# Performance work log

Hardware: AMD Instinct MI355X
Metric: run time of the kernel (lower is better)

The kernel has to match this reference:

```python
import jax, jax.numpy as jnp
import numpy as np

G, NPG, DEG = 64, 1024, 16          # graphs, nodes/graph, avg degree
N, E = G * NPG, G * NPG * DEG        # 65536 nodes, 1048576 edges
F, H = 128, 128                      # num_features, n_hidden
K1, K2 = NPG // 2, NPG // 4          # ceil(0.5*1024)=512, ceil(0.5*512)=256


def setup_inputs() -> dict:
    key = jax.random.key(0)
    ks = jax.random.split(key, 16)
    x = jax.random.normal(ks[0], (N, F), dtype=jnp.float32)
    # edges constrained within each graph (block-diagonal adjacency)
    offs = (jnp.arange(G, dtype=jnp.int32) * NPG)[:, None]
    src = (jax.random.randint(ks[1], (G, E // G), 0, NPG, dtype=jnp.int32) + offs).reshape(-1)
    dst = (jax.random.randint(ks[2], (G, E // G), 0, NPG, dtype=jnp.int32) + offs).reshape(-1)
    def lin(k, fi, fo):
        s = 1.0 / np.sqrt(fi)
        return jax.random.uniform(k, (fi, fo), jnp.float32, -s, s)
    return dict(
        x=x, src=src, dst=dst,
        W1=lin(ks[3], F, H),  b1=jnp.zeros((H,), jnp.float32),
        Ws1=lin(ks[4], H, 1), bs1=jnp.zeros((1,), jnp.float32),
        W2=lin(ks[5], H, H),  b2=jnp.zeros((H,), jnp.float32),
        Ws2=lin(ks[6], H, 1), bs2=jnp.zeros((1,), jnp.float32),
        Wl1=lin(ks[7], 2 * H, H), bl1=jnp.zeros((H,), jnp.float32),
        Wl2=lin(ks[8], H, 1),     bl2=jnp.zeros((1,), jnp.float32),
    )


def gcn_conv(x, src, dst, ew, W, b):
    """GCNConv: D^-1/2 (A+I) D^-1/2 (x W) + b, with edge weights ew."""
    n = x.shape[0]
    h = x @ W
    loop = jnp.arange(n, dtype=src.dtype)
    s = jnp.concatenate([src, loop])
    d = jnp.concatenate([dst, loop])
    w = jnp.concatenate([ew, jnp.ones((n,), x.dtype)])
    deg = jax.ops.segment_sum(w, d, num_segments=n)
    dinv = jnp.where(deg > 0, jax.lax.rsqrt(jnp.maximum(deg, 1e-12)), 0.0)
    norm = dinv[s] * dinv[d] * w
    return jax.ops.segment_sum(norm[:, None] * h[s], d, num_segments=n) + b


def sag_pool(x, src, dst, ew, Ws, bs, n_per_graph, k):
    """SAGPooling: GCN attention score, per-graph top-k, x*tanh(score), edge prune via mask."""
    n = x.shape[0]
    g = n // n_per_graph
    score = gcn_conv(x, src, dst, ew, Ws, bs)[:, 0]                 # [n]
    _, idx = jax.lax.top_k(score.reshape(g, n_per_graph), k)        # [g, k]
    perm = (idx + (jnp.arange(g, dtype=jnp.int32) * n_per_graph)[:, None]).reshape(-1)
    xn = x[perm] * jnp.tanh(score[perm])[:, None]                   # [g*k, H]
    kept = jnp.zeros((n,), bool).at[perm].set(True)
    nmap = jnp.zeros((n,), jnp.int32).at[perm].set(jnp.arange(g * k, dtype=jnp.int32))
    valid = kept[src] & kept[dst] & (ew > 0)
    ewn = jnp.where(valid, ew, 0.0)
    srcn = jnp.where(valid, nmap[src], 0)
    dstn = jnp.where(valid, nmap[dst], 0)
    return xn, srcn, dstn, ewn


def reference(x, src, dst, W1, b1, Ws1, bs1, W2, b2, Ws2, bs2, Wl1, bl1, Wl2, bl2):
    ew = jnp.ones((src.shape[0],), x.dtype)
    h = jax.nn.relu(gcn_conv(x, src, dst, ew, W1, b1))
    h, s1, d1, ew1 = sag_pool(h, src, dst, ew, Ws1, bs1, NPG, K1)
    hb = h.reshape(G, K1, H)
    x1 = jnp.concatenate([hb.max(axis=1), hb.mean(axis=1)], axis=1)  # [G, 2H]
    h = jax.nn.relu(gcn_conv(h, s1, d1, ew1, W2, b2))
    h, s2, d2, ew2 = sag_pool(h, s1, d1, ew1, Ws2, bs2, K1, K2)
    hb = h.reshape(G, K2, H)
    x2 = jnp.concatenate([hb.max(axis=1), hb.mean(axis=1)], axis=1)
    z = x1 + x2
    z = jax.nn.relu(z @ Wl1 + bl1)                                  # dropout: eval mode (identity)
    return (z @ Wl2 + bl2)[:, 0]                                     # [G]
```

## Files before the change

### kernel.cpp

```cpp
#include <hip/hip_runtime.h>
#include <math.h>

constexpr int NN1 = 65536;
constexpr int EE  = 1048576;
constexpr int GG  = 64;
constexpr int HH  = 128;
constexpr int NPG = 1024;
constexpr int EPG = 16384;
constexpr int K1  = 512;
constexpr int M1  = GG * K1;
constexpr int K2  = 256;
constexpr int M2  = GG * K2;

__device__ __forceinline__ float4 f4add(float4 a, float4 b)
{
    a.x += b.x; a.y += b.y; a.z += b.z; a.w += b.w; return a;
}

__global__ __launch_bounds__(256) void gemm_f32_128(const float* __restrict__ A,
                                                    const float* __restrict__ W,
                                                    const int* __restrict__ rbeg,
                                                    const int* __restrict__ rend,
                                                    float* __restrict__ C)
{
    __shared__ float Wl[64 * 160];
    const int t    = threadIdx.x;
    const int rowg = t >> 3;
    const int cg   = t & 7;
    const int r0   = (blockIdx.x << 7) + rowg;

    const float* Ar0 = A + ((size_t)r0 << 7);
    const float* Ar1 = Ar0 + (32 << 7);
    const float* Ar2 = Ar1 + (32 << 7);
    const float* Ar3 = Ar2 + (32 << 7);

    float acc[4][16];
#pragma unroll
    for (int i = 0; i < 4; ++i)
#pragma unroll
        for (int j = 0; j < 16; ++j) acc[i][j] = 0.f;

    {
        const float4* Wg = (const float4*)W;
#pragma unroll
        for (int i = 0; i < 8; ++i) {
            int idx = t + (i << 8);
            int k   = idx >> 5;
            int c4  = (idx & 31) << 2;
            *(float4*)&Wl[k * 160 + (c4 >> 4) * 20 + (c4 & 15)] = Wg[idx];
        }
    }
    float4 xc0 = *(const float4*)(Ar0), xc1 = *(const float4*)(Ar1);
    float4 xc2 = *(const float4*)(Ar2), xc3 = *(const float4*)(Ar3);
    __syncthreads();

    const float* wbase = &Wl[cg * 20];

#pragma unroll 1
    for (int k0 = 0; k0 < 64; k0 += 4) {
        float4 xn0 = *(const float4*)(Ar0 + k0 + 4);
        float4 xn1 = *(const float4*)(Ar1 + k0 + 4);
        float4 xn2 = *(const float4*)(Ar2 + k0 + 4);
        float4 xn3 = *(const float4*)(Ar3 + k0 + 4);
#pragma unroll
        for (int kk = 0; kk < 4; ++kk) {
            const float* wr = wbase + (k0 + kk) * 160;
            float x0 = ((const float*)&xc0)[kk], x1 = ((const float*)&xc1)[kk];
            float x2 = ((const float*)&xc2)[kk], x3 = ((const float*)&xc3)[kk];
#pragma unroll
            for (int jh = 0; jh < 16; jh += 8) {
                float wv[8];
                *(float4*)&wv[0] = *(const float4*)(wr + jh);
                *(float4*)&wv[4] = *(const float4*)(wr + jh + 4);
#pragma unroll
                for (int j = 0; j < 8; ++j) {
                    acc[0][jh + j] = fmaf(x0, wv[j], acc[0][jh + j]);
                    acc[1][jh + j] = fmaf(x1, wv[j], acc[1][jh + j]);
                    acc[2][jh + j] = fmaf(x2, wv[j], acc[2][jh + j]);
                    acc[3][jh + j] = fmaf(x3, wv[j], acc[3][jh + j]);
                }
            }
        }
        xc0 = xn0; xc1 = xn1; xc2 = xn2; xc3 = xn3;
    }
    __syncthreads();
    {
        const float4* Wg = (const float4*)(W + 64 * 128);
#pragma unroll
        for (int i = 0; i < 8; ++i) {
            int idx = t + (i << 8);
            int k   = idx >> 5;
            int c4  = (idx & 31) << 2;
            *(float4*)&Wl[k * 160 + (c4 >> 4) * 20 + (c4 & 15)] = Wg[idx];
        }
    }
    __syncthreads();

#pragma unroll 1
    for (int k0 = 64; k0 < 128; k0 += 4) {
        bool pf = (k0 < 124);
        float4 xn0, xn1, xn2, xn3;
        if (pf) {
            xn0 = *(const float4*)(Ar0 + k0 + 4);
            xn1 = *(const float4*)(Ar1 + k0 + 4);
            xn2 = *(const float4*)(Ar2 + k0 + 4);
            xn3 = *(const float4*)(Ar3 + k0 + 4);
        }
#pragma unroll
        for (int kk = 0; kk < 4; ++kk) {
            const float* wr = wbase + (k0 - 64 + kk) * 160;
            float x0 = ((const float*)&xc0)[kk], x1 = ((const float*)&xc1)[kk];
            float x2 = ((const float*)&xc2)[kk], x3 = ((const float*)&xc3)[kk];
#pragma unroll
            for (int jh = 0; jh < 16; jh += 8) {
                float wv[8];
                *(float4*)&wv[0] = *(const float4*)(wr + jh);
                *(float4*)&wv[4] = *(const float4*)(wr + jh + 4);
#pragma unroll
                for (int j = 0; j < 8; ++j) {
                    acc[0][jh + j] = fmaf(x0, wv[j], acc[0][jh + j]);
                    acc[1][jh + j] = fmaf(x1, wv[j], acc[1][jh + j]);
                    acc[2][jh + j] = fmaf(x2, wv[j], acc[2][jh + j]);
                    acc[3][jh + j] = fmaf(x3, wv[j], acc[3][jh + j]);
                }
            }
        }
        if (pf) { xc0 = xn0; xc1 = xn1; xc2 = xn2; xc3 = xn3; }
    }

#pragma unroll
    for (int i = 0; i < 4; ++i) {
        int r = r0 + (i << 5);
        float deg = (float)(rend[r] - rbeg[r]) + 1.0f;
        float sc = 1.0f / sqrtf(deg);
        float* cp = C + ((size_t)r << 7) + (cg << 4);
#pragma unroll
        for (int j = 0; j < 16; j += 4) {
            float4 v;
            v.x = acc[i][j] * sc; v.y = acc[i][j + 1] * sc;
            v.z = acc[i][j + 2] * sc; v.w = acc[i][j + 3] * sc;
            *(float4*)(cp + j) = v;
        }
    }
}

__global__ __launch_bounds__(1024) void build_csr1_k(const int* __restrict__ src, const int* __restrict__ dst,
                                                     int* __restrict__ rbeg, int* __restrict__ rend,
                                                     int* __restrict__ csr)
{
    __shared__ int cnt[NPG];
    int t = threadIdx.x, g = blockIdx.x;
    int ebase = g * EPG;
    cnt[t] = 0;
    __syncthreads();
#pragma unroll
    for (int k = 0; k < EPG / 1024; ++k) {
        int d = dst[ebase + t + k * 1024] & (NPG - 1);
        atomicAdd(&cnt[d], 1);
    }
    __syncthreads();
    int deg0 = cnt[t];
    int val = deg0;
    for (int off = 1; off < NPG; off <<= 1) {
        int u = (t >= off) ? cnt[t - off] : 0;
        __syncthreads();
        val += u; cnt[t] = val;
        __syncthreads();
    }
    int node = g * NPG + t;
    rbeg[node] = ebase + val - deg0;
    rend[node] = ebase + val;
    cnt[t] = val - deg0;
    __syncthreads();
#pragma unroll
    for (int k = 0; k < EPG / 1024; ++k) {
        int e = ebase + t + k * 1024;
        int d = dst[e] & (NPG - 1);
        int pos = atomicAdd(&cnt[d], 1);
        csr[ebase + pos] = src[e];
    }
}

__global__ __launch_bounds__(1024) void build_csr2_k(const int* __restrict__ src, const int* __restrict__ dst,
                                                     const int* __restrict__ nmap,
                                                     int* __restrict__ rbeg, int* __restrict__ rend,
                                                     int* __restrict__ csr)
{
    __shared__ int cnt[K1];
    int t = threadIdx.x, g = blockIdx.x;
    int ebase = g * EPG;
    if (t < K1) cnt[t] = 0;
    __syncthreads();
    int ns[EPG / 1024], nd[EPG / 1024];
#pragma unroll
    for (int k = 0; k < EPG / 1024; ++k) {
        int e = ebase + t + k * 1024;
        ns[k] = nmap[src[e]];
        nd[k] = nmap[dst[e]];
        if (ns[k] >= 0 && nd[k] >= 0) atomicAdd(&cnt[nd[k] & (K1 - 1)], 1);
    }
    __syncthreads();
    int deg0 = 0, val = 0;
    if (t < K1) { deg0 = cnt[t]; val = deg0; }
    for (int off = 1; off < K1; off <<= 1) {
        int u = (t < K1 && t >= off) ? cnt[t - off] : 0;
        __syncthreads();
        if (t < K1) { val += u; cnt[t] = val; }
        __syncthreads();
    }
    if (t < K1) {
        int node = g * K1 + t;
        rbeg[node] = ebase + val - deg0;
        rend[node] = ebase + val;
        cnt[t] = val - deg0;
    }
    __syncthreads();
#pragma unroll
    for (int k = 0; k < EPG / 1024; ++k) {
        if (ns[k] >= 0 && nd[k] >= 0) {
            int pos = atomicAdd(&cnt[nd[k] & (K1 - 1)], 1);
            csr[ebase + pos] = ns[k];
        }
    }
}

__global__ __launch_bounds__(256) void agg_feat_k(const float4* __restrict__ XWs,
                                                  const int* __restrict__ rbeg, const int* __restrict__ rend,
                                                  const int* __restrict__ csr,
                                                  const float* __restrict__ bias, const float* __restrict__ Ws,
                                                  float* __restrict__ hout, float* __restrict__ hss, int n)
{
    int nblk = gridDim.x;
    int bid  = blockIdx.x;
    int b    = (bid & 7) * (nblk >> 3) + (bid >> 3);
    int half = threadIdx.x >> 5;
    int lane = threadIdx.x & 31;
    int node = (b << 3) + half;
    if (node >= n) return;
    const float4* Xf = XWs + lane;

    float4 A = make_float4(0.f, 0.f, 0.f, 0.f), B = A, C = A, D = A;
    int p0 = rbeg[node], p1 = rend[node];
    int p = p0;
    for (; p + 8 <= p1; p += 8) {
        int s0 = csr[p], s1 = csr[p + 1], s2 = csr[p + 2], s3 = csr[p + 3];
        int s4 = csr[p + 4], s5 = csr[p + 5], s6 = csr[p + 6], s7 = csr[p + 7];
        float4 v0 = Xf[(size_t)s0 << 5], v1 = Xf[(size_t)s1 << 5];
        float4 v2 = Xf[(size_t)s2 << 5], v3 = Xf[(size_t)s3 << 5];
        float4 v4 = Xf[(size_t)s4 << 5], v5 = Xf[(size_t)s5 << 5];
        float4 v6 = Xf[(size_t)s6 << 5], v7 = Xf[(size_t)s7 << 5];
        A = f4add(A, v0); B = f4add(B, v1); C = f4add(C, v2); D = f4add(D, v3);
        A = f4add(A, v4); B = f4add(B, v5); C = f4add(C, v6); D = f4add(D, v7);
    }
    for (; p + 4 <= p1; p += 4) {
        int s0 = csr[p], s1 = csr[p + 1], s2 = csr[p + 2], s3 = csr[p + 3];
        float4 v0 = Xf[(size_t)s0 << 5], v1 = Xf[(size_t)s1 << 5];
        float4 v2 = Xf[(size_t)s2 << 5], v3 = Xf[(size_t)s3 << 5];
        A = f4add(A, v0); B = f4add(B, v1); C = f4add(C, v2); D = f4add(D, v3);
    }
    for (; p < p1; ++p) {
        int s = csr[p];
        A = f4add(A, Xf[(size_t)s << 5]);
    }
    float4 acc = f4add(f4add(A, B), f4add(C, D));
    acc = f4add(acc, Xf[(size_t)node << 5]);

    float dd = 1.0f / sqrtf((float)(p1 - p0) + 1.0f);
    float4 bb = *(const float4*)(bias + (lane << 2));
    acc.x = fmaxf(fmaf(acc.x, dd, bb.x), 0.f);
    acc.y = fmaxf(fmaf(acc.y, dd, bb.y), 0.f);
    acc.z = fmaxf(fmaf(acc.z, dd, bb.z), 0.f);
    acc.w = fmaxf(fmaf(acc.w, dd, bb.w), 0.f);
    *(float4*)(hout + ((size_t)node << 7) + (lane << 2)) = acc;

    float4 wsv = *(const float4*)(Ws + (lane << 2));
    float pq = acc.x * wsv.x + acc.y * wsv.y + acc.z * wsv.z + acc.w * wsv.w;
#pragma unroll
    for (int off = 16; off > 0; off >>= 1) pq += __shfl_down(pq, off, 32);
    if (lane == 0) hss[node] = dd * pq;
}

template <int NNE, int KK, bool MARK>
__global__ void sctopk_k(const int* __restrict__ rbeg, const int* __restrict__ rend,
                         const int* __restrict__ csr, const float* __restrict__ hss,
                         const float* __restrict__ bsp,
                         int* __restrict__ perm, float* __restrict__ tsel,
                         int* __restrict__ nmap)
{
    __shared__ unsigned long long keys[NNE];
    int t = threadIdx.x, g = blockIdx.x;
    int node = g * NNE + t;
    int p0 = rbeg[node], p1 = rend[node];
    float a = 0.f, b = 0.f, c = 0.f, e = 0.f;
    int p = p0;
    for (; p + 8 <= p1; p += 8) {
        int s0 = csr[p], s1 = csr[p + 1], s2 = csr[p + 2], s3 = csr[p + 3];
        int s4 = csr[p + 4], s5 = csr[p + 5], s6 = csr[p + 6], s7 = csr[p + 7];
        a += hss[s0]; b += hss[s1]; c += hss[s2]; e += hss[s3];
        a += hss[s4]; b += hss[s5]; c += hss[s6]; e += hss[s7];
    }
    for (; p + 4 <= p1; p += 4) {
        int s0 = csr[p], s1 = csr[p + 1], s2 = csr[p + 2], s3 = csr[p + 3];
        a += hss[s0]; b += hss[s1]; c += hss[s2]; e += hss[s3];
    }
    for (; p < p1; ++p) a += hss[csr[p]];
    float dd = 1.0f / sqrtf((float)(p1 - p0) + 1.0f);
    float s = fmaf((a + b) + (c + e) + hss[node], dd, bsp[0]);

    unsigned u = __float_as_uint(s);
    u = (u & 0x80000000u) ? ~u : (u | 0x80000000u);
    keys[t] = (((unsigned long long)u) << 32) | (unsigned)(NNE - 1 - t);
    __syncthreads();
    for (int k = 2; k <= NNE; k <<= 1) {
        for (int j = k >> 1; j > 0; j >>= 1) {
            int ixj = t ^ j;
            if (ixj > t) {
                unsigned long long ka = keys[t], kb = keys[ixj];
                bool up = ((t & k) == 0);
                if ((ka > kb) == up) { keys[t] = kb; keys[ixj] = ka; }
            }
            __syncthreads();
        }
    }
    unsigned long long key = keys[NNE - 1 - t];
    int idx = NNE - 1 - (int)(key & 0xFFFFFFFFu);
    if (t < KK) {
        perm[g * KK + t] = g * NNE + idx;
        unsigned uu = (unsigned)(key >> 32);
        float sc = __uint_as_float((uu & 0x80000000u) ? (uu ^ 0x80000000u) : ~uu);
        tsel[g * KK + t] = tanhf(sc);
        if (MARK) nmap[g * NNE + idx] = g * KK + t;
    } else if (MARK) {
        nmap[g * NNE + idx] = -1;
    }
}

__global__ void gather_k(const float* __restrict__ h, const float* __restrict__ tsel,
                         const int* __restrict__ perm, float* __restrict__ xn)
{
    int nblk = gridDim.x;
    int bid  = blockIdx.x;
    int b    = (bid & 7) * (nblk >> 3) + (bid >> 3);
    int gid = b * 256 + threadIdx.x;
    int node = gid >> 5, f4 = (gid & 31) << 2;
    int o = perm[node];
    float tv = tsel[node];
    float4 v = *(const float4*)(h + ((size_t)o << 7) + f4);
    v.x *= tv; v.y *= tv; v.z *= tv; v.w *= tv;
    *(float4*)(xn + ((size_t)node << 7) + f4) = v;
}

__global__ __launch_bounds__(128) void readout_p_k(const float* __restrict__ xn, float* __restrict__ part)
{
    int b = blockIdx.x, t = threadIdx.x;
    const float* bp = xn + (size_t)b * (128 * 128);
    float mx = -INFINITY, sm = 0.f;
#pragma unroll 4
    for (int r = 0; r < 128; ++r) {
        float v = bp[r * 128 + t];
        mx = fmaxf(mx, v);
        sm += v;
    }
    part[b * 256 + t] = mx;
    part[b * 256 + 128 + t] = sm;
}

__global__ __launch_bounds__(128) void mlp_k(const float* __restrict__ part1, const float* __restrict__ part2,
                                             const float* __restrict__ Wl1, const float* __restrict__ bl1,
                                             const float* __restrict__ Wl2, const float* __restrict__ bl2,
                                             float* __restrict__ out)
{
    __shared__ float z[256];
    __shared__ float red[128];
    int g = blockIdx.x, t = threadIdx.x;
    float mx1 = -INFINITY, sm1 = 0.f;
#pragma unroll
    for (int j = 0; j < 4; ++j) {
        mx1 = fmaxf(mx1, part1[(g * 4 + j) * 256 + t]);
        sm1 += part1[(g * 4 + j) * 256 + 128 + t];
    }
    float mx2 = -INFINITY, sm2 = 0.f;
#pragma unroll
    for (int j = 0; j < 2; ++j) {
        mx2 = fmaxf(mx2, part2[(g * 2 + j) * 256 + t]);
        sm2 += part2[(g * 2 + j) * 256 + 128 + t];
    }
    z[t]       = mx1 + mx2;
    z[t + 128] = sm1 * (1.f / 512.f) + sm2 * (1.f / 256.f);
    __syncthreads();
    float acc = bl1[t];
    for (int k = 0; k < 256; ++k) acc = fmaf(z[k], Wl1[k * 128 + t], acc);
    float zz = fmaxf(acc, 0.f);
    red[t] = zz * Wl2[t];
    __syncthreads();
    for (int off = 64; off > 0; off >>= 1) {
        if (t < off) red[t] += red[t + off];
        __syncthreads();
    }
    if (t == 0) out[g] = red[0] + bl2[0];
}

extern "C" void kernel_launch(void* const* d_in, const int* in_sizes, int n_in,
                              void* d_out, int out_size, void* d_ws, size_t ws_size,
                              hipStream_t stream)
{
    const float* x   = (const float*)d_in[0];
    const int*   src = (const int*)d_in[1];
    const int*   dst = (const int*)d_in[2];
    const float* W1  = (const float*)d_in[3];
    const float* b1  = (const float*)d_in[4];
    const float* Ws1 = (const float*)d_in[5];
    const float* bs1 = (const float*)d_in[6];
    const float* W2  = (const float*)d_in[7];
    const float* b2  = (const float*)d_in[8];
    const float* Ws2 = (const float*)d_in[9];
    const float* bs2 = (const float*)d_in[10];
    const float* Wl1 = (const float*)d_in[11];
    const float* bl1 = (const float*)d_in[12];
    const float* Wl2 = (const float*)d_in[13];
    const float* bl2 = (const float*)d_in[14];
    float* out = (float*)d_out;
    char* ws = (char*)d_ws;

    float* XW1 = (float*)(ws);
    float* h1  = (float*)(ws + ((size_t)32 << 20));
    float* xn  = XW1;
    float* XW2 = (float*)(ws + ((size_t)16 << 20));
    float* h2  = h1;
    float* xn2 = (float*)(ws + ((size_t)48 << 20));
    size_t SB = (size_t)64 << 20;
    auto alloc = [&](size_t bytes) { char* p = ws + SB; SB += (bytes + 255) & ~(size_t)255; return p; };
    int* csr1     = (int*)alloc((size_t)EE * 4);
    int* rbeg1    = (int*)alloc(NN1 * 4);
    int* rend1    = (int*)alloc(NN1 * 4);
    float* hss1   = (float*)alloc(NN1 * 4);
    int* nmap     = (int*)alloc(NN1 * 4);
    int* perm1    = (int*)alloc(M1 * 4);
    float* tsel1  = (float*)alloc(M1 * 4);
    int* rbeg2    = (int*)alloc(M1 * 4);
    int* rend2    = (int*)alloc(M1 * 4);
    float* hss2   = (float*)alloc(M1 * 4);
    int* perm2    = (int*)alloc(M2 * 4);
    float* tsel2  = (float*)alloc(M2 * 4);
    float* part1  = (float*)alloc(256 * 256 * 4);
    float* part2  = (float*)alloc(128 * 256 * 4);
    int* csr2     = csr1;
    (void)ws_size; (void)in_sizes; (void)n_in; (void)out_size;

    build_csr1_k<<<GG, 1024, 0, stream>>>(src, dst, rbeg1, rend1, csr1);
    gemm_f32_128<<<NN1 / 128, 256, 0, stream>>>(x, W1, rbeg1, rend1, XW1);
    agg_feat_k<<<NN1 / 8, 256, 0, stream>>>((const float4*)XW1, rbeg1, rend1, csr1, b1, Ws1, h1, hss1, NN1);
    sctopk_k<NPG, K1, true><<<GG, NPG, 0, stream>>>(rbeg1, rend1, csr1, hss1, bs1, perm1, tsel1, nmap);
    gather_k<<<(M1 * 32) / 256, 256, 0, stream>>>(h1, tsel1, perm1, xn);
    readout_p_k<<<M1 / 128, 128, 0, stream>>>(xn, part1);
    build_csr2_k<<<GG, 1024, 0, stream>>>(src, dst, nmap, rbeg2, rend2, csr2);
    gemm_f32_128<<<M1 / 128, 256, 0, stream>>>(xn, W2, rbeg2, rend2, XW2);
    agg_feat_k<<<M1 / 8, 256, 0, stream>>>((const float4*)XW2, rbeg2, rend2, csr2, b2, Ws2, h2, hss2, M1);
    sctopk_k<K1, K2, false><<<GG, K1, 0, stream>>>(rbeg2, rend2, csr2, hss2, bs2, perm2, tsel2, nullptr);
    gather_k<<<(M2 * 32) / 256, 256, 0, stream>>>(h2, tsel2, perm2, xn2);
    readout_p_k<<<M2 / 128, 128, 0, stream>>>(xn2, part2);
    mlp_k<<<GG, 128, 0, stream>>>(part1, part2, Wl1, bl1, Wl2, bl2, out);
}
```

Measured before the change: 219.5 us.

## Fuse top-k gather and tanh scaling into second GEMM and readout kernels

Removes the standalone gather kernels that materialized the pooled feature matrices. The second-layer GEMM now reads rows of h1 indirectly through perm1 and applies the tanh score factor in its epilogue. The readout kernels also gather through perm and apply tsel on the fly. This saves two launches and a write and reread of the pooled matrices, at the cost of indirect row loads in the GEMM and readout and redundant gathers of h1 by two kernels.

```diff
diff --git a/kernel.cpp b/kernel.cpp
--- a/kernel.cpp
+++ b/kernel.cpp
@@ -17,11 +17,11 @@
     a.x += b.x; a.y += b.y; a.z += b.z; a.w += b.w; return a;
 }
 
-__global__ __launch_bounds__(256) void gemm_f32_128(const float* __restrict__ A,
-                                                    const float* __restrict__ W,
-                                                    const int* __restrict__ rbeg,
-                                                    const int* __restrict__ rend,
-                                                    float* __restrict__ C)
+__global__ __launch_bounds__(256) void gemm1_k(const float* __restrict__ A,
+                                               const float* __restrict__ W,
+                                               const int* __restrict__ rbeg,
+                                               const int* __restrict__ rend,
+                                               float* __restrict__ C)
 {
     __shared__ float Wl[64 * 160];
     const int t    = threadIdx.x;
@@ -133,6 +133,135 @@
         int r = r0 + (i << 5);
         float deg = (float)(rend[r] - rbeg[r]) + 1.0f;
         float sc = 1.0f / sqrtf(deg);
+        float* cp = C + ((size_t)r << 7) + (cg << 4);
+#pragma unroll
+        for (int j = 0; j < 16; j += 4) {
+            float4 v;
+            v.x = acc[i][j] * sc; v.y = acc[i][j + 1] * sc;
+            v.z = acc[i][j + 2] * sc; v.w = acc[i][j + 3] * sc;
+            *(float4*)(cp + j) = v;
+        }
+    }
+}
+
+__global__ __launch_bounds__(256) void gemm2_k(const float* __restrict__ A,
+                                               const float* __restrict__ W,
+                                               const int* __restrict__ rbeg,
+                                               const int* __restrict__ rend,
+                                               const int* __restrict__ perm,
+                                               const float* __restrict__ tsel,
+                                               float* __restrict__ C)
+{
+    __shared__ float Wl[64 * 160];
+    const int t    = threadIdx.x;
+    const int rowg = t >> 3;
+    const int cg   = t & 7;
+    const int r0   = (blockIdx.x << 7) + rowg;
+
+    const float* Ar0 = A + ((size_t)perm[r0] << 7);
+    const float* Ar1 = A + ((size_t)perm[r0 + 32] << 7);
+    const float* Ar2 = A + ((size_t)perm[r0 + 64] << 7);
+    const float* Ar3 = A + ((size_t)perm[r0 + 96] << 7);
+
+    float acc[4][16];
+#pragma unroll
+    for (int i = 0; i < 4; ++i)
+#pragma unroll
+        for (int j = 0; j < 16; ++j) acc[i][j] = 0.f;
+
+    {
+        const float4* Wg = (const float4*)W;
+#pragma unroll
+        for (int i = 0; i < 8; ++i) {
+            int idx = t + (i << 8);
+            int k   = idx >> 5;
+            int c4  = (idx & 31) << 2;
+            *(float4*)&Wl[k * 160 + (c4 >> 4) * 20 + (c4 & 15)] = Wg[idx];
+        }
+    }
+    float4 xc0 = *(const float4*)(Ar0), xc1 = *(const float4*)(Ar1);
+    float4 xc2 = *(const float4*)(Ar2), xc3 = *(const float4*)(Ar3);
+    __syncthreads();
+
+    const float* wbase = &Wl[cg * 20];
+
+#pragma unroll 1
+    for (int k0 = 0; k0 < 64; k0 += 4) {
+        float4 xn0 = *(const float4*)(Ar0 + k0 + 4);
+        float4 xn1 = *(const float4*)(Ar1 + k0 + 4);
+        float4 xn2 = *(const float4*)(Ar2 + k0 + 4);
+        float4 xn3 = *(const float4*)(Ar3 + k0 + 4);
+#pragma unroll
+        for (int kk = 0; kk < 4; ++kk) {
+            const float* wr = wbase + (k0 + kk) * 160;
+            float x0 = ((const float*)&xc0)[kk], x1 = ((const float*)&xc1)[kk];
+            float x2 = ((const float*)&xc2)[kk], x3 = ((const float*)&xc3)[kk];
+#pragma unroll
+            for (int jh = 0; jh < 16; jh += 8) {
+                float wv[8];
+                *(float4*)&wv[0] = *(const float4*)(wr + jh);
+                *(float4*)&wv[4] = *(const float4*)(wr + jh + 4);
+#pragma unroll
+                for (int j = 0; j < 8; ++j) {
+                    acc[0][jh + j] = fmaf(x0, wv[j], acc[0][jh + j]);
+                    acc[1][jh + j] = fmaf(x1, wv[j], acc[1][jh + j]);
+                    acc[2][jh + j] = fmaf(x2, wv[j], acc[2][jh + j]);
+                    acc[3][jh + j] = fmaf(x3, wv[j], acc[3][jh + j]);
+                }
+            }
+        }
+        xc0 = xn0; xc1 = xn1; xc2 = xn2; xc3 = xn3;
+    }
+    __syncthreads();
+    {
+        const float4* Wg = (const float4*)(W + 64 * 128);
+#pragma unroll
+        for (int i = 0; i < 8; ++i) {
+            int idx = t + (i << 8);
+            int k   = idx >> 5;
+            int c4  = (idx & 31) << 2;
+            *(float4*)&Wl[k * 160 + (c4 >> 4) * 20 + (c4 & 15)] = Wg[idx];
+        }
+    }
+    __syncthreads();
+
+#pragma unroll 1
+    for (int k0 = 64; k0 < 128; k0 += 4) {
+        bool pf = (k0 < 124);
+        float4 xn0, xn1, xn2, xn3;
+        if (pf) {
+            xn0 = *(const float4*)(Ar0 + k0 + 4);
+            xn1 = *(const float4*)(Ar1 + k0 + 4);
+            xn2 = *(const float4*)(Ar2 + k0 + 4);
+            xn3 = *(const float4*)(Ar3 + k0 + 4);
+        }
+#pragma unroll
+        for (int kk = 0; kk < 4; ++kk) {
+            const float* wr = wbase + (k0 - 64 + kk) * 160;
+            float x0 = ((const float*)&xc0)[kk], x1 = ((const float*)&xc1)[kk];
+            float x2 = ((const float*)&xc2)[kk], x3 = ((const float*)&xc3)[kk];
+#pragma unroll
+            for (int jh = 0; jh < 16; jh += 8) {
+                float wv[8];
+                *(float4*)&wv[0] = *(const float4*)(wr + jh);
+                *(float4*)&wv[4] = *(const float4*)(wr + jh + 4);
+#pragma unroll
+                for (int j = 0; j < 8; ++j) {
+                    acc[0][jh + j] = fmaf(x0, wv[j], acc[0][jh + j]);
+                    acc[1][jh + j] = fmaf(x1, wv[j], acc[1][jh + j]);
+                    acc[2][jh + j] = fmaf(x2, wv[j], acc[2][jh + j]);
+                    acc[3][jh + j] = fmaf(x3, wv[j], acc[3][jh + j]);
+                }
+            }
+        }
+        if (pf) { xc0 = xn0; xc1 = xn1; xc2 = xn2; xc3 = xn3; }
+    }
+
+#pragma unroll
+    for (int i = 0; i < 4; ++i) {
+        int r = r0 + (i << 5);
+        float deg = (float)(rend[r] - rbeg[r]) + 1.0f;
+        float sc = tsel[r] / sqrtf(deg);
         float* cp = C + ((size_t)r << 7) + (cg << 4);
 #pragma unroll
         for (int j = 0; j < 16; j += 4) {
@@ -335,29 +464,19 @@
     }
 }
 
-__global__ void gather_k(const float* __restrict__ h, const float* __restrict__ tsel,
-                         const int* __restrict__ perm, float* __restrict__ xn)
-{
-    int nblk = gridDim.x;
-    int bid  = blockIdx.x;
-    int b    = (bid & 7) * (nblk >> 3) + (bid >> 3);
-    int gid = b * 256 + threadIdx.x;
-    int node = gid >> 5, f4 = (gid & 31) << 2;
-    int o = perm[node];
-    float tv = tsel[node];
-    float4 v = *(const float4*)(h + ((size_t)o << 7) + f4);
-    v.x *= tv; v.y *= tv; v.z *= tv; v.w *= tv;
-    *(float4*)(xn + ((size_t)node << 7) + f4) = v;
-}
-
-__global__ __launch_bounds__(128) void readout_p_k(const float* __restrict__ xn, float* __restrict__ part)
+__global__ __launch_bounds__(128) void readout_ix_k(const float* __restrict__ h,
+                                                    const int* __restrict__ perm,
+                                                    const float* __restrict__ tsel,
+                                                    float* __restrict__ part)
 {
     int b = blockIdx.x, t = threadIdx.x;
-    const float* bp = xn + (size_t)b * (128 * 128);
+    int base = b * 128;
     float mx = -INFINITY, sm = 0.f;
 #pragma unroll 4
     for (int r = 0; r < 128; ++r) {
-        float v = bp[r * 128 + t];
+        int o = perm[base + r];
+        float tv = tsel[base + r];
+        float v = h[((size_t)o << 7) + t] * tv;
         mx = fmaxf(mx, v);
         sm += v;
     }
@@ -424,10 +543,8 @@
 
     float* XW1 = (float*)(ws);
     float* h1  = (float*)(ws + ((size_t)32 << 20));
-    float* xn  = XW1;
-    float* XW2 = (float*)(ws + ((size_t)16 << 20));
-    float* h2  = h1;
-    float* xn2 = (float*)(ws + ((size_t)48 << 20));
+    float* XW2 = (float*)(ws);
+    float* h2  = (float*)(ws + ((size_t)16 << 20));
     size_t SB = (size_t)64 << 20;
     auto alloc = [&](size_t bytes) { char* p = ws + SB; SB += (bytes + 255) & ~(size_t)255; return p; };
     int* csr1     = (int*)alloc((size_t)EE * 4);
@@ -448,16 +565,14 @@
     (void)ws_size; (void)in_sizes; (void)n_in; (void)out_size;
 
     build_csr1_k<<<GG, 1024, 0, stream>>>(src, dst, rbeg1, rend1, csr1);
-    gemm_f32_128<<<NN1 / 128, 256, 0, stream>>>(x, W1, rbeg1, rend1, XW1);
+    gemm1_k<<<NN1 / 128, 256, 0, stream>>>(x, W1, rbeg1, rend1, XW1);
     agg_feat_k<<<NN1 / 8, 256, 0, stream>>>((const float4*)XW1, rbeg1, rend1, csr1, b1, Ws1, h1, hss1, NN1);
     sctopk_k<NPG, K1, true><<<GG, NPG, 0, stream>>>(rbeg1, rend1, csr1, hss1, bs1, perm1, tsel1, nmap);
-    gather_k<<<(M1 * 32) / 256, 256, 0, stream>>>(h1, tsel1, perm1, xn);
-    readout_p_k<<<M1 / 128, 128, 0, stream>>>(xn, part1);
     build_csr2_k<<<GG, 1024, 0, stream>>>(src, dst, nmap, rbeg2, rend2, csr2);
-    gemm_f32_128<<<M1 / 128, 256, 0, stream>>>(xn, W2, rbeg2, rend2, XW2);
+    gemm2_k<<<M1 / 128, 256, 0, stream>>>(h1, W2, rbeg2, rend2, perm1, tsel1, XW2);
+    readout_ix_k<<<M1 / 128, 128, 0, stream>>>(h1, perm1, tsel1, part1);
     agg_feat_k<<<M1 / 8, 256, 0, stream>>>((const float4*)XW2, rbeg2, rend2, csr2, b2, Ws2, h2, hss2, M1);
     sctopk_k<K1, K2, false><<<GG, K1, 0, stream>>>(rbeg2, rend2, csr2, hss2, bs2, perm2, tsel2, nullptr);
-    gather_k<<<(M2 * 32) / 256, 256, 0, stream>>>(h2, tsel2, perm2, xn2);
-    readout_p_k<<<M2 / 128, 128, 0, stream>>>(xn2, part2);
+    readout_ix_k<<<M2 / 128, 128, 0, stream>>>(h2, perm2, tsel2, part2);
     mlp_k<<<GG, 128, 0, stream>>>(part1, part2, Wl1, bl1, Wl2, bl2, out);
 }
```

Measured after the change: 216.2 us. Within noise of the previous version (-1.5%).
